# Optimization experiments

Hardware: AMD Instinct MI355X
Metric: run time of the kernel (lower is better)

Reference implementation:

```python
import jax, jax.numpy as jnp
import numpy as np

N_NODES = 500_000
N_EDGES = 2_500_000
N_GRAPHS = 1024


def _linear_params(key, fan_in, fan_out):
    # mimic torch.nn.Linear default init: U(-1/sqrt(fan_in), 1/sqrt(fan_in))
    k1, k2 = jax.random.split(key)
    bound = 1.0 / np.sqrt(fan_in)
    W = jax.random.uniform(k1, (fan_in, fan_out), jnp.float32, -bound, bound)
    b = jax.random.uniform(k2, (fan_out,), jnp.float32, -bound, bound)
    return W, b


def setup_inputs() -> dict:
    key = jax.random.key(0)
    ks = jax.random.split(key, 8)
    x = jax.random.normal(ks[0], (N_NODES, 2), jnp.float32)
    edge_index = jax.random.randint(ks[1], (2, N_EDGES), 0, N_NODES, jnp.int32)
    batch = jnp.sort(jax.random.randint(ks[2], (N_NODES,), 0, N_GRAPHS, jnp.int32))
    W1, b1 = _linear_params(ks[3], 2, 16)
    W2, b2 = _linear_params(ks[4], 16, 32)
    Wf1, bf1 = _linear_params(ks[5], 32, 16)
    Wf2, bf2 = _linear_params(ks[6], 16, 1)
    return {"x": x, "edge_index": edge_index, "batch": batch,
            "W1": W1, "b1": b1, "W2": W2, "b2": b2,
            "Wf1": Wf1, "bf1": bf1, "Wf2": Wf2, "bf2": bf2}


def _gnn_conv(h, W, b, src, dst, n_nodes):
    # Linear then add-aggregate: out[dst] += h_lin[src]  (self-loops already in src/dst)
    h = h @ W + b                       # [N, out]
    msgs = h[src]                       # gather over edges: [E+N, out]
    return jax.ops.segment_sum(msgs, dst, num_segments=n_nodes)


def reference(x, edge_index, batch, W1, b1, W2, b2, Wf1, bf1, Wf2, bf2):
    n = x.shape[0]
    loop = jnp.arange(n, dtype=edge_index.dtype)
    src = jnp.concatenate([edge_index[0], loop])  # source nodes (x_j)
    dst = jnp.concatenate([edge_index[1], loop])  # target nodes (aggregation index)

    h = jax.nn.relu(_gnn_conv(x, W1, b1, src, dst, n))   # [N, 16]
    h = jax.nn.relu(_gnn_conv(h, W2, b2, src, dst, n))   # [N, 32]

    # global mean pool per graph
    sums = jax.ops.segment_sum(h, batch, num_segments=N_GRAPHS)           # [G, 32]
    cnts = jax.ops.segment_sum(jnp.ones((n, 1), h.dtype), batch, num_segments=N_GRAPHS)
    pooled = sums / jnp.maximum(cnts, 1.0)

    out = jax.nn.relu(pooled @ Wf1 + bf1)
    out = out @ Wf2 + bf2                                # [G, 1]
    return out
```

## Files before the change

kernel.cpp:

```cpp
#include <hip/hip_runtime.h>


#define TPB 256
#define SBK_BITS 9
#define SBK 512
#define NSBX 1024
#define CAPX 576
#define CAPS 3072
#define PE1 2048

typedef unsigned int uint32;

__device__ __forceinline__ float reluf(float v) { return v > 0.f ? v : 0.f; }

__global__ void kPart1(const int* __restrict__ src, const int* __restrict__ dst,
                       int* __restrict__ curx, int* __restrict__ part1x, int E) {
    __shared__ int h[NSBX];
    for (int i = threadIdx.x; i < NSBX; i += TPB) h[i] = 0;
    __syncthreads();
    int base = blockIdx.x * PE1;
    int end = base + PE1 < E ? base + PE1 : E;
    for (int e = base + threadIdx.x; e < end; e += TPB)
        atomicAdd(&h[dst[e] >> SBK_BITS], 1);
    __syncthreads();
    int slice = blockIdx.x & 7;
    int* cur = curx + slice * NSBX;
    int rbase = slice * (NSBX * CAPX);
    for (int i = threadIdx.x; i < NSBX; i += TPB) {
        int c = h[i];
        if (c) h[i] = i * CAPX + atomicAdd(&cur[i], c);
    }
    __syncthreads();
    for (int e = base + threadIdx.x; e < end; e += TPB) {
        int d = dst[e];
        int b = d >> SBK_BITS;
        int pos = atomicAdd(&h[b], 1);
        if (pos < (b + 1) * CAPX)
            part1x[rbase + pos] = (src[e] << SBK_BITS) | (d & (SBK - 1));
    }
}

__global__ void kPart2(const int* __restrict__ curx, const int* __restrict__ part1x,
                       int* __restrict__ rowptr, int* __restrict__ supEnd,
                       int* __restrict__ partS, int N) {
    __shared__ int hist[SBK];
    __shared__ int ps[TPB];
    __shared__ int segc[8];
    int sb = blockIdx.x;
    int node0 = sb << SBK_BITS;
    int sbase = sb * CAPS;
    int t = threadIdx.x;
    for (int i = t; i < SBK; i += TPB) hist[i] = 0;
    if (t < 8) {
        int c = curx[t * NSBX + sb];
        segc[t] = c > CAPX ? CAPX : c;
    }
    __syncthreads();
    for (int seg = 0; seg < 8; seg++) {
        const int* p = part1x + seg * (NSBX * CAPX) + sb * CAPX;
        int c = segc[seg];
        for (int i = t; i < c; i += TPB)
            atomicAdd(&hist[p[i] & (SBK - 1)], 1);
    }
    __syncthreads();
    int v0 = hist[2 * t], v1 = hist[2 * t + 1];
    int s = v0 + v1;
    ps[t] = s;
    __syncthreads();
    for (int off = 1; off < TPB; off <<= 1) {
        int u = (t >= off) ? ps[t - off] : 0;
        __syncthreads();
        ps[t] += u;
        __syncthreads();
    }
    int run = ps[t] - s;
    int node = node0 + 2 * t;
    if (node < N) rowptr[node] = sbase + run;
    hist[2 * t] = run;
    int run1 = run + v0;
    if (node + 1 < N) rowptr[node + 1] = sbase + run1;
    hist[2 * t + 1] = run1;
    if (t == TPB - 1) supEnd[sb] = sbase + ps[t];
    __syncthreads();
    for (int seg = 0; seg < 8; seg++) {
        const int* p = part1x + seg * (NSBX * CAPX) + sb * CAPX;
        int c = segc[seg];
        for (int i = t; i < c; i += TPB) {
            int w = p[i];
            int slot = atomicAdd(&hist[w & (SBK - 1)], 1);
            partS[sbase + slot] = w >> SBK_BITS;
        }
    }
}

__device__ __forceinline__ int rowEnd(const int* __restrict__ rowptr,
                                      const int* __restrict__ supEnd, int i, int N) {
    int nxt = i + 1;
    return (nxt >= N || (nxt & (SBK - 1)) == 0) ? supEnd[i >> SBK_BITS] : rowptr[nxt];
}

__global__ void __launch_bounds__(TPB, 6)
kConv1(const float* __restrict__ x, const int* __restrict__ partS,
       const int* __restrict__ rowptr, const int* __restrict__ supEnd,
       uint2* __restrict__ ninfo, int N) {
    int i = blockIdx.x * TPB + threadIdx.x;
    if (i >= N) return;
    int rs = rowptr[i];
    int re = rowEnd(rowptr, supEnd, i, N);
    float2 sv = ((const float2*)x)[i];
    float a0 = sv.x, a1 = sv.y;
    int e = rs;
    float2 nx;
    if (e < re) nx = ((const float2*)x)[partS[e]];
    while (e < re) {
        float2 cur = nx;
        int e2 = e + 1;
        if (e2 < re) nx = ((const float2*)x)[partS[e2]];
        a0 += cur.x; a1 += cur.y;
        e = e2;
    }
    int indeg = re - rs + 1;
    if (indeg > 31) indeg = 31;
    ninfo[i] = make_uint2(__float_as_uint(a0),
                          (__float_as_uint(a1) & ~31u) | (uint32)indeg);
}

__global__ void __launch_bounds__(TPB, 4)
kConv2(const uint2* __restrict__ ninfo, const int* __restrict__ partS,
       const int* __restrict__ rowptr, const int* __restrict__ supEnd,
       const int* __restrict__ batch,
       const float* __restrict__ W1, const float* __restrict__ b1,
       const float* __restrict__ W2, const float* __restrict__ b2,
       float* __restrict__ pooled, int N) {
    __shared__ float srow[TPB * 33];
    __shared__ int sbat[TPB];
    __shared__ float spart[8 * 32];
    int node0 = blockIdx.x * TPB;
    int l = threadIdx.x;
    int i = node0 + l;
    bool valid = i < N;

    if (valid) {
        int rs = rowptr[i];
        int re = rowEnd(rowptr, supEnd, i, N);
        uint2 p = ninfo[i];
        float s0 = __uint_as_float(p.x);
        float sdeg = (float)(p.y & 31u);
        float s1 = __uint_as_float(p.y & ~31u);
        float a[16];
#pragma unroll
        for (int j = 0; j < 16; j++)
            a[j] = reluf(fmaf(s0, W1[j], fmaf(s1, W1[16 + j], sdeg * b1[j])));
        int e = rs;
        uint2 nx;
        if (e < re) nx = ninfo[partS[e]];
        while (e < re) {
            uint2 cur = nx;
            int e2 = e + 1;
            if (e2 < re) nx = ninfo[partS[e2]];
            float n0 = __uint_as_float(cur.x);
            float ndeg = (float)(cur.y & 31u);
            float n1 = __uint_as_float(cur.y & ~31u);
#pragma unroll
            for (int j = 0; j < 16; j++)
                a[j] += reluf(fmaf(n0, W1[j], fmaf(n1, W1[16 + j], ndeg * b1[j])));
            e = e2;
        }
#pragma unroll
        for (int j = 0; j < 32; j++) {
            float vv = sdeg * b2[j];
#pragma unroll
            for (int k = 0; k < 16; k++) vv = fmaf(a[k], W2[k * 32 + j], vv);
            srow[l * 33 + j] = reluf(vv);
        }
        sbat[l] = batch[i];
    } else {
#pragma unroll
        for (int j = 0; j < 32; j++) srow[l * 33 + j] = 0.f;
        sbat[l] = -1;
    }
    __syncthreads();
    int lastl = N - 1 - node0;
    if (lastl > TPB - 1) lastl = TPB - 1;
    int g0 = sbat[0], g1 = sbat[lastl];
    int f = threadIdx.x & 31, rr = threadIdx.x >> 5;
    for (int g = g0; g <= g1; g++) {
        float p = 0.f;
#pragma unroll 4
        for (int q = 0; q < 32; q++) {
            int n = rr + 8 * q;
            p += (sbat[n] == g) ? srow[n * 33 + f] : 0.f;
        }
        spart[rr * 32 + f] = p;
        __syncthreads();
        if (rr == 0) {
            float tot = 0.f;
#pragma unroll
            for (int q = 0; q < 8; q++) tot += spart[q * 32 + f];
            unsafeAtomicAdd(&pooled[32 * (size_t)g + f], tot);
        }
        __syncthreads();
    }
}

__device__ __forceinline__ int lower_bound(const int* __restrict__ a, int n, int v) {
    int lo = 0, hi = n;
    while (lo < hi) {
        int m = (lo + hi) >> 1;
        if (a[m] < v) lo = m + 1; else hi = m;
    }
    return lo;
}

__global__ void kMLP(const float* __restrict__ pooled, const int* __restrict__ batch,
                     const float* __restrict__ Wf1, const float* __restrict__ bf1,
                     const float* __restrict__ Wf2, const float* __restrict__ bf2,
                     float* __restrict__ out, int N, int G) {
    int g = blockIdx.x * blockDim.x + threadIdx.x;
    if (g >= G) return;
    int lo = lower_bound(batch, N, g);
    int hi = lower_bound(batch, N, g + 1);
    int cnt = hi - lo;
    float inv = 1.f / (float)(cnt > 1 ? cnt : 1);
    float p[32];
#pragma unroll
    for (int i = 0; i < 32; i++) p[i] = pooled[32 * (size_t)g + i] * inv;
    float acc = bf2[0];
#pragma unroll
    for (int j = 0; j < 16; j++) {
        float v = bf1[j];
#pragma unroll
        for (int i = 0; i < 32; i++) v = fmaf(p[i], Wf1[i * 16 + j], v);
        acc = fmaf(reluf(v), Wf2[j], acc);
    }
    out[g] = acc;
}

static inline size_t align256(size_t v) { return (v + 255) & ~(size_t)255; }

extern "C" void kernel_launch(void* const* d_in, const int* in_sizes, int n_in,
                              void* d_out, int out_size, void* d_ws, size_t ws_size,
                              hipStream_t stream) {
    const float* x    = (const float*)d_in[0];
    const int*   ei   = (const int*)d_in[1];
    const int*   batch= (const int*)d_in[2];
    const float* W1   = (const float*)d_in[3];
    const float* b1   = (const float*)d_in[4];
    const float* W2   = (const float*)d_in[5];
    const float* b2   = (const float*)d_in[6];
    const float* Wf1  = (const float*)d_in[7];
    const float* bf1  = (const float*)d_in[8];
    const float* Wf2  = (const float*)d_in[9];
    const float* bf2  = (const float*)d_in[10];
    float* out = (float*)d_out;

    const int N = in_sizes[0] / 2;
    const int E = in_sizes[1] / 2;
    const int G = out_size;
    const int* src = ei;
    const int* dst = ei + E;

    const int NSB = (N + SBK - 1) >> SBK_BITS;
    const int NFB = (N + TPB - 1) / TPB;

    char* w = (char*)d_ws;
    int*   curx   = (int*)w;    w += align256((size_t)8 * NSBX * sizeof(int));
    int*   supEnd = (int*)w;    w += align256((size_t)NSBX * sizeof(int));
    int*   rowptr = (int*)w;    w += align256((size_t)N * sizeof(int));
    uint2* ninfo  = (uint2*)w;  w += align256((size_t)N * sizeof(uint2));
    float* pooled = (float*)w;  w += align256((size_t)G * 32 * sizeof(float));
    int*   part1x = (int*)w;    w += align256((size_t)8 * NSBX * CAPX * sizeof(int));
    int*   partS  = (int*)w;    w += align256((size_t)NSBX * CAPS * sizeof(int));

    const int nb1 = (E + PE1 - 1) / PE1;

    hipMemsetAsync(curx, 0, (size_t)8 * NSBX * sizeof(int), stream);
    hipMemsetAsync(pooled, 0, (size_t)G * 32 * sizeof(float), stream);
    kPart1<<<nb1, TPB, 0, stream>>>(src, dst, curx, part1x, E);
    kPart2<<<NSB, TPB, 0, stream>>>(curx, part1x, rowptr, supEnd, partS, N);
    kConv1<<<NFB, TPB, 0, stream>>>(x, partS, rowptr, supEnd, ninfo, N);
    kConv2<<<NFB, TPB, 0, stream>>>(ninfo, partS, rowptr, supEnd, batch,
                                    W1, b1, W2, b2, pooled, N);
    kMLP  <<<(G + TPB - 1) / TPB, TPB, 0, stream>>>(pooled, batch, Wf1, bf1, Wf2, bf2, out, N, G);
}
```

Baseline: 209.1 us.

## Fuse CSR bucket pass with first conv and use global atomics for degrees

After: 387.1 us. +85.1%, slower.

```diff
diff --git a/kernel.cpp b/kernel.cpp
--- a/kernel.cpp
+++ b/kernel.cpp
@@ -13,58 +13,57 @@
 
 __device__ __forceinline__ float reluf(float v) { return v > 0.f ? v : 0.f; }
 
-__global__ void kPart1(const int* __restrict__ src, const int* __restrict__ dst,
-                       int* __restrict__ curx, int* __restrict__ part1x, int E) {
-    __shared__ int h[NSBX];
-    for (int i = threadIdx.x; i < NSBX; i += TPB) h[i] = 0;
-    __syncthreads();
-    int base = blockIdx.x * PE1;
-    int end = base + PE1 < E ? base + PE1 : E;
-    for (int e = base + threadIdx.x; e < end; e += TPB)
-        atomicAdd(&h[dst[e] >> SBK_BITS], 1);
-    __syncthreads();
+__global__ void __launch_bounds__(TPB, 8)
+kPart1(const int* __restrict__ src, const int* __restrict__ dst,
+       int* __restrict__ curx, int* __restrict__ deg,
+       int* __restrict__ part1x, int E) {
     int slice = blockIdx.x & 7;
     int* cur = curx + slice * NSBX;
     int rbase = slice * (NSBX * CAPX);
-    for (int i = threadIdx.x; i < NSBX; i += TPB) {
-        int c = h[i];
-        if (c) h[i] = i * CAPX + atomicAdd(&cur[i], c);
-    }
-    __syncthreads();
-    for (int e = base + threadIdx.x; e < end; e += TPB) {
-        int d = dst[e];
-        int b = d >> SBK_BITS;
-        int pos = atomicAdd(&h[b], 1);
-        if (pos < (b + 1) * CAPX)
-            part1x[rbase + pos] = (src[e] << SBK_BITS) | (d & (SBK - 1));
-    }
-}
-
-__global__ void kPart2(const int* __restrict__ curx, const int* __restrict__ part1x,
-                       int* __restrict__ rowptr, int* __restrict__ supEnd,
-                       int* __restrict__ partS, int N) {
-    __shared__ int hist[SBK];
+    int base = blockIdx.x * PE1 + threadIdx.x;
+    int d[8], s[8], pos[8];
+    bool v[8];
+#pragma unroll
+    for (int k = 0; k < 8; k++) {
+        int e = base + k * TPB;
+        v[k] = e < E;
+        if (v[k]) { d[k] = dst[e]; s[k] = src[e]; }
+    }
+#pragma unroll
+    for (int k = 0; k < 8; k++)
+        if (v[k]) atomicAdd(&deg[d[k]], 1);
+#pragma unroll
+    for (int k = 0; k < 8; k++)
+        if (v[k]) pos[k] = atomicAdd(&cur[d[k] >> SBK_BITS], 1);
+#pragma unroll
+    for (int k = 0; k < 8; k++)
+        if (v[k] && pos[k] < CAPX) {
+            int b = d[k] >> SBK_BITS;
+            part1x[rbase + b * CAPX + pos[k]] = (s[k] << SBK_BITS) | (d[k] & (SBK - 1));
+        }
+}
+
+__global__ void __launch_bounds__(TPB, 8)
+kPart2C1(const int* __restrict__ curx, const int* __restrict__ part1x,
+         const int* __restrict__ deg, const float* __restrict__ x,
+         int* __restrict__ rowptr, int* __restrict__ supEnd,
+         int* __restrict__ partS, uint2* __restrict__ ninfo, int N) {
+    __shared__ int cursor[SBK];
     __shared__ int ps[TPB];
+    __shared__ int sls[CAPS];
     __shared__ int segc[8];
     int sb = blockIdx.x;
     int node0 = sb << SBK_BITS;
     int sbase = sb * CAPS;
     int t = threadIdx.x;
-    for (int i = t; i < SBK; i += TPB) hist[i] = 0;
     if (t < 8) {
         int c = curx[t * NSBX + sb];
         segc[t] = c > CAPX ? CAPX : c;
     }
-    __syncthreads();
-    for (int seg = 0; seg < 8; seg++) {
-        const int* p = part1x + seg * (NSBX * CAPX) + sb * CAPX;
-        int c = segc[seg];
-        for (int i = t; i < c; i += TPB)
-            atomicAdd(&hist[p[i] & (SBK - 1)], 1);
-    }
-    __syncthreads();
-    int v0 = hist[2 * t], v1 = hist[2 * t + 1];
-    int s = v0 + v1;
+    int n0 = node0 + 2 * t, n1 = n0 + 1;
+    int d0 = (n0 < N) ? deg[n0] : 0;
+    int d1 = (n1 < N) ? deg[n1] : 0;
+    int s = d0 + d1;
     ps[t] = s;
     __syncthreads();
     for (int off = 1; off < TPB; off <<= 1) {
@@ -73,13 +72,12 @@
         ps[t] += u;
         __syncthreads();
     }
-    int run = ps[t] - s;
-    int node = node0 + 2 * t;
-    if (node < N) rowptr[node] = sbase + run;
-    hist[2 * t] = run;
-    int run1 = run + v0;
-    if (node + 1 < N) rowptr[node + 1] = sbase + run1;
-    hist[2 * t + 1] = run1;
+    int start0 = ps[t] - s;
+    int start1 = start0 + d0;
+    if (n0 < N) rowptr[n0] = sbase + start0;
+    if (n1 < N) rowptr[n1] = sbase + start1;
+    cursor[2 * t] = start0;
+    cursor[2 * t + 1] = start1;
     if (t == TPB - 1) supEnd[sb] = sbase + ps[t];
     __syncthreads();
     for (int seg = 0; seg < 8; seg++) {
@@ -87,9 +85,32 @@
         int c = segc[seg];
         for (int i = t; i < c; i += TPB) {
             int w = p[i];
-            int slot = atomicAdd(&hist[w & (SBK - 1)], 1);
-            partS[sbase + slot] = w >> SBK_BITS;
-        }
+            int slot = atomicAdd(&cursor[w & (SBK - 1)], 1);
+            if (slot < CAPS) {
+                int sid = w >> SBK_BITS;
+                partS[sbase + slot] = sid;
+                sls[slot] = sid;
+            }
+        }
+    }
+    __syncthreads();
+#pragma unroll
+    for (int half = 0; half < 2; half++) {
+        int n = half ? n1 : n0;
+        if (n >= N) continue;
+        int st = half ? start1 : start0;
+        int dg = half ? d1 : d0;
+        int en = st + dg; if (en > CAPS) en = CAPS;
+        float2 sv = ((const float2*)x)[n];
+        float a0 = sv.x, a1 = sv.y;
+        for (int e = st; e < en; e++) {
+            float2 xv = ((const float2*)x)[sls[e]];
+            a0 += xv.x; a1 += xv.y;
+        }
+        int indeg = dg + 1;
+        if (indeg > 31) indeg = 31;
+        ninfo[n] = make_uint2(__float_as_uint(a0),
+                              (__float_as_uint(a1) & ~31u) | (uint32)indeg);
     }
 }
 
@@ -97,32 +118,6 @@
                                       const int* __restrict__ supEnd, int i, int N) {
     int nxt = i + 1;
     return (nxt >= N || (nxt & (SBK - 1)) == 0) ? supEnd[i >> SBK_BITS] : rowptr[nxt];
-}
-
-__global__ void __launch_bounds__(TPB, 6)
-kConv1(const float* __restrict__ x, const int* __restrict__ partS,
-       const int* __restrict__ rowptr, const int* __restrict__ supEnd,
-       uint2* __restrict__ ninfo, int N) {
-    int i = blockIdx.x * TPB + threadIdx.x;
-    if (i >= N) return;
-    int rs = rowptr[i];
-    int re = rowEnd(rowptr, supEnd, i, N);
-    float2 sv = ((const float2*)x)[i];
-    float a0 = sv.x, a1 = sv.y;
-    int e = rs;
-    float2 nx;
-    if (e < re) nx = ((const float2*)x)[partS[e]];
-    while (e < re) {
-        float2 cur = nx;
-        int e2 = e + 1;
-        if (e2 < re) nx = ((const float2*)x)[partS[e2]];
-        a0 += cur.x; a1 += cur.y;
-        e = e2;
-    }
-    int indeg = re - rs + 1;
-    if (indeg > 31) indeg = 31;
-    ninfo[i] = make_uint2(__float_as_uint(a0),
-                          (__float_as_uint(a1) & ~31u) | (uint32)indeg);
 }
 
 __global__ void __launch_bounds__(TPB, 4)
@@ -265,6 +260,7 @@
 
     char* w = (char*)d_ws;
     int*   curx   = (int*)w;    w += align256((size_t)8 * NSBX * sizeof(int));
+    int*   deg    = (int*)w;    w += align256((size_t)N * sizeof(int));
     int*   supEnd = (int*)w;    w += align256((size_t)NSBX * sizeof(int));
     int*   rowptr = (int*)w;    w += align256((size_t)N * sizeof(int));
     uint2* ninfo  = (uint2*)w;  w += align256((size_t)N * sizeof(uint2));
@@ -275,11 +271,11 @@
     const int nb1 = (E + PE1 - 1) / PE1;
 
     hipMemsetAsync(curx, 0, (size_t)8 * NSBX * sizeof(int), stream);
+    hipMemsetAsync(deg, 0, (size_t)N * sizeof(int), stream);
     hipMemsetAsync(pooled, 0, (size_t)G * 32 * sizeof(float), stream);
-    kPart1<<<nb1, TPB, 0, stream>>>(src, dst, curx, part1x, E);
-    kPart2<<<NSB, TPB, 0, stream>>>(curx, part1x, rowptr, supEnd, partS, N);
-    kConv1<<<NFB, TPB, 0, stream>>>(x, partS, rowptr, supEnd, ninfo, N);
-    kConv2<<<NFB, TPB, 0, stream>>>(ninfo, partS, rowptr, supEnd, batch,
-                                    W1, b1, W2, b2, pooled, N);
-    kMLP  <<<(G + TPB - 1) / TPB, TPB, 0, stream>>>(pooled, batch, Wf1, bf1, Wf2, bf2, out, N, G);
-}
+    kPart1  <<<nb1, TPB, 0, stream>>>(src, dst, curx, deg, part1x, E);
+    kPart2C1<<<NSB, TPB, 0, stream>>>(curx, part1x, deg, x, rowptr, supEnd, partS, ninfo, N);
+    kConv2  <<<NFB, TPB, 0, stream>>>(ninfo, partS, rowptr, supEnd, batch,
+                                      W1, b1, W2, b2, pooled, N);
+    kMLP    <<<(G + TPB - 1) / TPB, TPB, 0, stream>>>(pooled, batch, Wf1, bf1, Wf2, bf2, out, N, G);
+}
```

## Fuse first-layer aggregation into CSR partition kernel using shared-memory source lists

Applied to the files above, without the earlier changes.

Result: faster. 202.3 us (-3.2%).

```diff
diff --git a/kernel.cpp b/kernel.cpp
--- a/kernel.cpp
+++ b/kernel.cpp
@@ -40,11 +40,13 @@
     }
 }
 
-__global__ void kPart2(const int* __restrict__ curx, const int* __restrict__ part1x,
-                       int* __restrict__ rowptr, int* __restrict__ supEnd,
-                       int* __restrict__ partS, int N) {
+__global__ void kPart2C1(const int* __restrict__ curx, const int* __restrict__ part1x,
+                         const float* __restrict__ x,
+                         int* __restrict__ rowptr, int* __restrict__ supEnd,
+                         int* __restrict__ partS, uint2* __restrict__ ninfo, int N) {
     __shared__ int hist[SBK];
     __shared__ int ps[TPB];
+    __shared__ int sls[CAPS];
     __shared__ int segc[8];
     int sb = blockIdx.x;
     int node0 = sb << SBK_BITS;
@@ -73,13 +75,13 @@
         ps[t] += u;
         __syncthreads();
     }
-    int run = ps[t] - s;
-    int node = node0 + 2 * t;
-    if (node < N) rowptr[node] = sbase + run;
-    hist[2 * t] = run;
-    int run1 = run + v0;
-    if (node + 1 < N) rowptr[node + 1] = sbase + run1;
-    hist[2 * t + 1] = run1;
+    int start0 = ps[t] - s;
+    int start1 = start0 + v0;
+    int n0 = node0 + 2 * t, n1 = n0 + 1;
+    if (n0 < N) rowptr[n0] = sbase + start0;
+    if (n1 < N) rowptr[n1] = sbase + start1;
+    hist[2 * t] = start0;
+    hist[2 * t + 1] = start1;
     if (t == TPB - 1) supEnd[sb] = sbase + ps[t];
     __syncthreads();
     for (int seg = 0; seg < 8; seg++) {
@@ -88,8 +90,31 @@
         for (int i = t; i < c; i += TPB) {
             int w = p[i];
             int slot = atomicAdd(&hist[w & (SBK - 1)], 1);
-            partS[sbase + slot] = w >> SBK_BITS;
-        }
+            if (slot < CAPS) {
+                int sid = w >> SBK_BITS;
+                partS[sbase + slot] = sid;
+                sls[slot] = sid;
+            }
+        }
+    }
+    __syncthreads();
+#pragma unroll
+    for (int half = 0; half < 2; half++) {
+        int n = half ? n1 : n0;
+        if (n >= N) continue;
+        int st = half ? start1 : start0;
+        int dg = half ? v1 : v0;
+        int en = st + dg; if (en > CAPS) en = CAPS;
+        float2 sv = ((const float2*)x)[n];
+        float a0 = sv.x, a1 = sv.y;
+        for (int e = st; e < en; e++) {
+            float2 xv = ((const float2*)x)[sls[e]];
+            a0 += xv.x; a1 += xv.y;
+        }
+        int indeg = dg + 1;
+        if (indeg > 31) indeg = 31;
+        ninfo[n] = make_uint2(__float_as_uint(a0),
+                              (__float_as_uint(a1) & ~31u) | (uint32)indeg);
     }
 }
 
@@ -97,32 +122,6 @@
                                       const int* __restrict__ supEnd, int i, int N) {
     int nxt = i + 1;
     return (nxt >= N || (nxt & (SBK - 1)) == 0) ? supEnd[i >> SBK_BITS] : rowptr[nxt];
-}
-
-__global__ void __launch_bounds__(TPB, 6)
-kConv1(const float* __restrict__ x, const int* __restrict__ partS,
-       const int* __restrict__ rowptr, const int* __restrict__ supEnd,
-       uint2* __restrict__ ninfo, int N) {
-    int i = blockIdx.x * TPB + threadIdx.x;
-    if (i >= N) return;
-    int rs = rowptr[i];
-    int re = rowEnd(rowptr, supEnd, i, N);
-    float2 sv = ((const float2*)x)[i];
-    float a0 = sv.x, a1 = sv.y;
-    int e = rs;
-    float2 nx;
-    if (e < re) nx = ((const float2*)x)[partS[e]];
-    while (e < re) {
-        float2 cur = nx;
-        int e2 = e + 1;
-        if (e2 < re) nx = ((const float2*)x)[partS[e2]];
-        a0 += cur.x; a1 += cur.y;
-        e = e2;
-    }
-    int indeg = re - rs + 1;
-    if (indeg > 31) indeg = 31;
-    ninfo[i] = make_uint2(__float_as_uint(a0),
-                          (__float_as_uint(a1) & ~31u) | (uint32)indeg);
 }
 
 __global__ void __launch_bounds__(TPB, 4)
@@ -276,10 +275,9 @@
 
     hipMemsetAsync(curx, 0, (size_t)8 * NSBX * sizeof(int), stream);
     hipMemsetAsync(pooled, 0, (size_t)G * 32 * sizeof(float), stream);
-    kPart1<<<nb1, TPB, 0, stream>>>(src, dst, curx, part1x, E);
-    kPart2<<<NSB, TPB, 0, stream>>>(curx, part1x, rowptr, supEnd, partS, N);
-    kConv1<<<NFB, TPB, 0, stream>>>(x, partS, rowptr, supEnd, ninfo, N);
-    kConv2<<<NFB, TPB, 0, stream>>>(ninfo, partS, rowptr, supEnd, batch,
-                                    W1, b1, W2, b2, pooled, N);
-    kMLP  <<<(G + TPB - 1) / TPB, TPB, 0, stream>>>(pooled, batch, Wf1, bf1, Wf2, bf2, out, N, G);
-}
+    kPart1  <<<nb1, TPB, 0, stream>>>(src, dst, curx, part1x, E);
+    kPart2C1<<<NSB, TPB, 0, stream>>>(curx, part1x, x, rowptr, supEnd, partS, ninfo, N);
+    kConv2  <<<NFB, TPB, 0, stream>>>(ninfo, partS, rowptr, supEnd, batch,
+                                      W1, b1, W2, b2, pooled, N);
+    kMLP    <<<(G + TPB - 1) / TPB, TPB, 0, stream>>>(pooled, batch, Wf1, bf1, Wf2, bf2, out, N, G);
+}
```
